# Kernel optimization log

Measured on AMD Instinct MI355X. Metric: run time of the kernel, lower is better.

The kernel has to match this reference:

```python
import jax, jax.numpy as jnp
import numpy as np

N = 32768      # total nodes (512 graphs x 64 padded nodes)
E = 262144     # edges (avg degree 8)
F_IN = 74      # atom feature dim
D0 = 128       # dim_embedding
D1 = 256       # hidden feats
B = 512        # batch_size (graphs)
NPG = 64       # nodes per graph
EPS = 1e-5     # BatchNorm1d eps


def setup_inputs() -> dict:
    key = jax.random.key(0)
    ks = jax.random.split(key, 8)
    def rn(k, shape, s=0.05):
        return jax.random.normal(k, shape, jnp.float32) * s
    # init_transform weight [D0, F_IN]; padding=True zeroes the last row
    W_init = rn(ks[0], (D0, F_IN)).at[-1].set(0.0)
    return {
        "node_feats": jax.random.normal(ks[1], (N, F_IN), jnp.float32),
        "W_init": W_init,
        "gcn_w1": rn(ks[2], (D0, D1)), "gcn_b1": jnp.zeros((D1,), jnp.float32),
        "res_w1": rn(ks[3], (D1, D0)), "res_b1": jnp.zeros((D1,), jnp.float32),
        "bn_g1": jnp.ones((D1,), jnp.float32), "bn_b1": jnp.zeros((D1,), jnp.float32),
        "gcn_w2": rn(ks[4], (D1, D1)), "gcn_b2": jnp.zeros((D1,), jnp.float32),
        "bn_g2": jnp.ones((D1,), jnp.float32), "bn_b2": jnp.zeros((D1,), jnp.float32),
        "edge_src": jax.random.randint(ks[5], (E,), 0, N),
        "edge_dst": jax.random.randint(ks[6], (E,), 0, N),
    }


def _agg(x, src, dst):
    # DGL GraphConv norm='both': D_out^{-1/2} gather-scatter D_in^{-1/2}, degrees clamped to >= 1
    ones = jnp.ones((src.shape[0],), x.dtype)
    deg_out = jnp.clip(jax.ops.segment_sum(ones, src, num_segments=N), 1.0)
    deg_in = jnp.clip(jax.ops.segment_sum(ones, dst, num_segments=N), 1.0)
    xs = x * jax.lax.rsqrt(deg_out)[:, None]
    agg = jax.ops.segment_sum(xs[src], dst, num_segments=N)  # [N, d]
    return agg * jax.lax.rsqrt(deg_in)[:, None]


def _bn(x, g, b):
    # BatchNorm1d training-mode: batch stats over node axis, biased var
    m = x.mean(0)
    v = x.var(0)
    return (x - m) * jax.lax.rsqrt(v + EPS) * g + b


def reference(node_feats, W_init, gcn_w1, gcn_b1, res_w1, res_b1, bn_g1, bn_b1,
              gcn_w2, gcn_b2, bn_g2, bn_b2, edge_src, edge_dst):
    h = node_feats @ W_init.T  # [N, D0]
    # layer 1: residual Linear 128->256, GCN(aggregate then weight, since in<out), GELU, BN
    res = h @ res_w1.T + res_b1
    g = jax.nn.gelu(_agg(h, edge_src, edge_dst) @ gcn_w1 + gcn_b1, approximate=False)
    h = _bn(g + res, bn_g1, bn_b1)
    # layer 2: Identity residual
    g = jax.nn.gelu(_agg(h, edge_src, edge_dst) @ gcn_w2 + gcn_b2, approximate=False)
    h = _bn(g + h, bn_g2, bn_b2)
    return h.reshape(B, NPG, D1)
```

## Files before the change

kernel.cpp:

```cpp
#include <hip/hip_runtime.h>
#include <hip/hip_bf16.h>
#include <math.h>

#define N_NODES 32768
#define E_EDGES 262144
#define F_INF   74
#define D0      128
#define D1      256
#define BN_EPS  1e-5f
#define RBLK    1024

typedef float f32x4 __attribute__((ext_vector_type(4)));
typedef short s16x8 __attribute__((ext_vector_type(8)));

__device__ __forceinline__ float b2f(ushort h) { return __uint_as_float(((unsigned)h) << 16); }
__device__ __forceinline__ ushort f2b(float f) {
    unsigned u = __float_as_uint(f);
    return (ushort)((u + 0x7FFFu + ((u >> 16) & 1u)) >> 16);
}
__device__ __forceinline__ float gelu_exact(float x) {
    return 0.5f * x * (1.0f + erff(x * 0.70710678118654752440f));
}


__global__ void k_degrees(const int* __restrict__ src, const int* __restrict__ dst,
                          int* __restrict__ deg) {
    int e = blockIdx.x * 256 + threadIdx.x;
    if (e < E_EDGES) {
        atomicAdd(&deg[src[e]], 1);
        atomicAdd(&deg[N_NODES + dst[e]], 1);
    }
}

__global__ __launch_bounds__(1024) void k_scan(const int* __restrict__ deg,
                                               int* __restrict__ row_off,
                                               float* __restrict__ rsq_out,
                                               float* __restrict__ rsq_in,
                                               int* __restrict__ cursor) {
    __shared__ int part[1024];
    int t = threadIdx.x;
    int base = t * 32;
    int loc[32];
    int s = 0;
    #pragma unroll
    for (int i = 0; i < 32; i++) { loc[i] = s; s += deg[N_NODES + base + i]; }
    part[t] = s;
    #pragma unroll
    for (int i = 0; i < 32; i++) {
        int n = base + i;
        int d_o = deg[n];           if (d_o < 1) d_o = 1;
        int d_i = deg[N_NODES + n]; if (d_i < 1) d_i = 1;
        rsq_out[n] = 1.0f / sqrtf((float)d_o);
        rsq_in[n]  = 1.0f / sqrtf((float)d_i);
        cursor[n] = 0;
    }
    __syncthreads();
    for (int off = 1; off < 1024; off <<= 1) {
        int v = 0;
        if (t >= off) v = part[t - off];
        __syncthreads();
        if (t >= off) part[t] += v;
        __syncthreads();
    }
    int pre = (t == 0) ? 0 : part[t - 1];
    #pragma unroll
    for (int i = 0; i < 32; i++) row_off[base + i] = pre + loc[i];
    if (t == 1023) row_off[N_NODES] = part[1023];
}

__global__ void k_fill(const int* __restrict__ src, const int* __restrict__ dst,
                       const int* __restrict__ row_off, int* __restrict__ cursor,
                       int* __restrict__ csr_src) {
    int e = blockIdx.x * 256 + threadIdx.x;
    if (e < E_EDGES) {
        int d = dst[e];
        int slot = atomicAdd(&cursor[d], 1);
        csr_src[row_off[d] + slot] = src[e];
    }
}

__global__ void k_prep(const float* __restrict__ Wi, const float* __restrict__ w1,
                       const float* __restrict__ rw, const float* __restrict__ w2,
                       float* __restrict__ WT, ushort* __restrict__ WB1,
                       ushort* __restrict__ RWB, ushort* __restrict__ WB2) {
    int idx = blockIdx.x * 256 + threadIdx.x;
    {
        int n = idx >> 8, k = idx & 255;
        WB2[idx] = f2b(w2[k * D1 + n]);
    }
    if (idx < D1 * D0) {
        int n = idx >> 7, k = idx & 127;
        WB1[idx] = f2b(w1[k * D1 + n]);
        RWB[idx] = f2b(rw[idx]);
    }
    if (idx < F_INF * D0) {
        int f = idx / D0, c = idx % D0;
        WT[f * D0 + c] = Wi[c * F_INF + f];
    }
}


__global__ __launch_bounds__(256) void k_init_gemm(
    const float* __restrict__ nf, const float* __restrict__ WT,
    ushort* __restrict__ h0) {
    __shared__ float sNF[64 * 76];
    int nb = blockIdx.x * 64;
    int tid = threadIdx.x;
    for (int idx = tid; idx < 64 * F_INF; idx += 256) {
        int row = idx / F_INF, f = idx % F_INF;
        sNF[row * 76 + f] = nf[(size_t)nb * F_INF + idx];
    }
    __syncthreads();
    int tc = tid & 31;
    int tn = tid >> 5;
    int c0 = tc * 4;
    float acc[8][4];
    #pragma unroll
    for (int i = 0; i < 8; i++)
        #pragma unroll
        for (int j = 0; j < 4; j++) acc[i][j] = 0.f;
    for (int k = 0; k < F_INF; k++) {
        float4 w = *reinterpret_cast<const float4*>(&WT[k * D0 + c0]);
        #pragma unroll
        for (int i = 0; i < 8; i++) {
            float a = sNF[(tn * 8 + i) * 76 + k];
            acc[i][0] += a * w.x; acc[i][1] += a * w.y;
            acc[i][2] += a * w.z; acc[i][3] += a * w.w;
        }
    }
    #pragma unroll
    for (int i = 0; i < 8; i++) {
        ushort4 o;
        o.x = f2b(acc[i][0]); o.y = f2b(acc[i][1]);
        o.z = f2b(acc[i][2]); o.w = f2b(acc[i][3]);
        *reinterpret_cast<ushort4*>(&h0[(size_t)(nb + tn * 8 + i) * D0 + c0]) = o;
    }
}


__global__ __launch_bounds__(512) void k_layer1f(
    const ushort* __restrict__ h0B,
    const float* __restrict__ rsq_out, const float* __restrict__ rsq_in,
    const int* __restrict__ row_off, const int* __restrict__ csr_src,
    const ushort* __restrict__ WB1, const ushort* __restrict__ RWB,
    const float* __restrict__ b1, const float* __restrict__ rb,
    ushort* __restrict__ t1B, float* __restrict__ partials) {
    __shared__ ushort sA[32 * 128];
    int tid = threadIdx.x;
    int rbase = blockIdx.x * 32;
    {
        int nloc = tid >> 4;
        int node = rbase + nloc;
        int f = (tid & 15) * 8;
        int beg = row_off[node], end = row_off[node + 1];
        float a[8];
        #pragma unroll
        for (int j = 0; j < 8; j++) a[j] = 0.f;
        int e = beg;
        for (; e + 3 < end; e += 4) {
            int s0 = csr_src[e], s1 = csr_src[e + 1], s2 = csr_src[e + 2], s3 = csr_src[e + 3];
            float c0 = rsq_out[s0], c1 = rsq_out[s1], c2 = rsq_out[s2], c3 = rsq_out[s3];
            s16x8 v0 = *reinterpret_cast<const s16x8*>(&h0B[(size_t)s0 * D0 + f]);
            s16x8 v1 = *reinterpret_cast<const s16x8*>(&h0B[(size_t)s1 * D0 + f]);
            s16x8 v2 = *reinterpret_cast<const s16x8*>(&h0B[(size_t)s2 * D0 + f]);
            s16x8 v3 = *reinterpret_cast<const s16x8*>(&h0B[(size_t)s3 * D0 + f]);
            #pragma unroll
            for (int j = 0; j < 8; j++)
                a[j] += b2f((ushort)v0[j]) * c0 + b2f((ushort)v1[j]) * c1 +
                        b2f((ushort)v2[j]) * c2 + b2f((ushort)v3[j]) * c3;
        }
        for (; e < end; e++) {
            int s = csr_src[e];
            float sc = rsq_out[s];
            s16x8 v = *reinterpret_cast<const s16x8*>(&h0B[(size_t)s * D0 + f]);
            #pragma unroll
            for (int j = 0; j < 8; j++) a[j] += b2f((ushort)v[j]) * sc;
        }
        float si = rsq_in[node];
        s16x8 o;
        #pragma unroll
        for (int j = 0; j < 8; j++) o[j] = (short)f2b(a[j] * si);
        int boff = nloc * 256 + ((f * 2) ^ ((nloc & 15) << 4));
        *reinterpret_cast<s16x8*>(((char*)sA) + boff) = o;
    }
    __syncthreads();
    int w = tid >> 6, lane = tid & 63, m = lane & 15, g4 = lane >> 4;
    int cb = w * 32;
    s16x8 BG[2][4], BR[2][4];
    #pragma unroll
    for (int nt = 0; nt < 2; nt++)
        #pragma unroll
        for (int j = 0; j < 4; j++) {
            BG[nt][j] = *reinterpret_cast<const s16x8*>(&WB1[(size_t)(cb + nt * 16 + m) * D0 + j * 32 + g4 * 8]);
            BR[nt][j] = *reinterpret_cast<const s16x8*>(&RWB[(size_t)(cb + nt * 16 + m) * D0 + j * 32 + g4 * 8]);
        }
    float bg[2], brv[2];
    #pragma unroll
    for (int nt = 0; nt < 2; nt++) {
        bg[nt]  = b1[cb + nt * 16 + m];
        brv[nt] = rb[cb + nt * 16 + m];
    }
    float ps[2] = {0.f, 0.f}, pq[2] = {0.f, 0.f};
    #pragma unroll
    for (int rt = 0; rt < 2; rt++) {
        int row = rt * 16 + m;
        s16x8 aA[4], aH[4];
        #pragma unroll
        for (int j = 0; j < 4; j++) {
            int boff = row * 256 + (((j * 4 + g4) * 16) ^ ((row & 15) << 4));
            aA[j] = *reinterpret_cast<const s16x8*>(((const char*)sA) + boff);
            aH[j] = *reinterpret_cast<const s16x8*>(&h0B[(size_t)(rbase + row) * D0 + j * 32 + g4 * 8]);
        }
        f32x4 accG[2], accR[2];
        #pragma unroll
        for (int nt = 0; nt < 2; nt++) {
            accG[nt] = (f32x4){0.f, 0.f, 0.f, 0.f};
            accR[nt] = (f32x4){0.f, 0.f, 0.f, 0.f};
        }
        #pragma unroll
        for (int j = 0; j < 4; j++)
            #pragma unroll
            for (int nt = 0; nt < 2; nt++) {
                accG[nt] = __builtin_amdgcn_mfma_f32_16x16x32_bf16(aA[j], BG[nt][j], accG[nt], 0, 0, 0);
                accR[nt] = __builtin_amdgcn_mfma_f32_16x16x32_bf16(aH[j], BR[nt][j], accR[nt], 0, 0, 0);
            }
        #pragma unroll
        for (int nt = 0; nt < 2; nt++) {
            int col = cb + nt * 16 + m;
            #pragma unroll
            for (int r = 0; r < 4; r++) {
                int orow = rbase + rt * 16 + g4 * 4 + r;
                float v = gelu_exact(accG[nt][r] + bg[nt]) + accR[nt][r] + brv[nt];
                t1B[(size_t)orow * D1 + col] = f2b(v);
                ps[nt] += v; pq[nt] += v * v;
            }
        }
    }
    #pragma unroll
    for (int nt = 0; nt < 2; nt++) {
        float s = ps[nt], q = pq[nt];
        s += __shfl_xor(s, 16); s += __shfl_xor(s, 32);
        q += __shfl_xor(q, 16); q += __shfl_xor(q, 32);
        if (g4 == 0) {
            int col = cb + nt * 16 + m;
            partials[(size_t)col * RBLK + blockIdx.x] = s;
            partials[(size_t)(256 + col) * RBLK + blockIdx.x] = q;
        }
    }
}


__global__ __launch_bounds__(512) void k_layer2f(
    const ushort* __restrict__ t1B,
    const float* __restrict__ sc1, const float* __restrict__ sh1,
    const float* __restrict__ rsq_out, const float* __restrict__ rsq_in,
    const int* __restrict__ row_off, const int* __restrict__ csr_src,
    const ushort* __restrict__ WB2, const float* __restrict__ b2,
    ushort* __restrict__ t2B, float* __restrict__ partials) {
    __shared__ ushort sA[32 * 256];
    int tid = threadIdx.x;
    int rbase = blockIdx.x * 32;
    {
        int nloc = tid >> 4;
        int node = rbase + nloc;
        int f0 = (tid & 15) * 8;
        int beg = row_off[node], end = row_off[node + 1];
        float a0[8], a1[8];
        #pragma unroll
        for (int j = 0; j < 8; j++) { a0[j] = 0.f; a1[j] = 0.f; }
        float ssum = 0.f;
        int e = beg;
        for (; e + 1 < end; e += 2) {
            int s0 = csr_src[e], s1 = csr_src[e + 1];
            float c0 = rsq_out[s0], c1 = rsq_out[s1];
            s16x8 v00 = *reinterpret_cast<const s16x8*>(&t1B[(size_t)s0 * D1 + f0]);
            s16x8 v01 = *reinterpret_cast<const s16x8*>(&t1B[(size_t)s0 * D1 + f0 + 128]);
            s16x8 v10 = *reinterpret_cast<const s16x8*>(&t1B[(size_t)s1 * D1 + f0]);
            s16x8 v11 = *reinterpret_cast<const s16x8*>(&t1B[(size_t)s1 * D1 + f0 + 128]);
            ssum += c0 + c1;
            #pragma unroll
            for (int j = 0; j < 8; j++) {
                a0[j] += b2f((ushort)v00[j]) * c0 + b2f((ushort)v10[j]) * c1;
                a1[j] += b2f((ushort)v01[j]) * c0 + b2f((ushort)v11[j]) * c1;
            }
        }
        for (; e < end; e++) {
            int s = csr_src[e];
            float sc = rsq_out[s];
            s16x8 v0 = *reinterpret_cast<const s16x8*>(&t1B[(size_t)s * D1 + f0]);
            s16x8 v1 = *reinterpret_cast<const s16x8*>(&t1B[(size_t)s * D1 + f0 + 128]);
            ssum += sc;
            #pragma unroll
            for (int j = 0; j < 8; j++) {
                a0[j] += b2f((ushort)v0[j]) * sc;
                a1[j] += b2f((ushort)v1[j]) * sc;
            }
        }
        float si = rsq_in[node];
        s16x8 o0, o1;
        #pragma unroll
        for (int j = 0; j < 8; j++) {
            o0[j] = (short)f2b((sc1[f0 + j] * a0[j] + sh1[f0 + j] * ssum) * si);
            o1[j] = (short)f2b((sc1[f0 + 128 + j] * a1[j] + sh1[f0 + 128 + j] * ssum) * si);
        }
        int swz = (nloc & 15) << 4;
        int b0 = nloc * 512 + ((f0 * 2) ^ swz);
        int b1_ = nloc * 512 + (((f0 + 128) * 2) ^ swz);
        *reinterpret_cast<s16x8*>(((char*)sA) + b0) = o0;
        *reinterpret_cast<s16x8*>(((char*)sA) + b1_) = o1;
    }
    __syncthreads();
    int w = tid >> 6, lane = tid & 63, m = lane & 15, g4 = lane >> 4;
    int cb = w * 32;
    s16x8 BG[2][8];
    #pragma unroll
    for (int nt = 0; nt < 2; nt++)
        #pragma unroll
        for (int j = 0; j < 8; j++)
            BG[nt][j] = *reinterpret_cast<const s16x8*>(&WB2[(size_t)(cb + nt * 16 + m) * D1 + j * 32 + g4 * 8]);
    float bg[2], a1c[2], s1c[2];
    #pragma unroll
    for (int nt = 0; nt < 2; nt++) {
        int col = cb + nt * 16 + m;
        bg[nt] = b2[col]; a1c[nt] = sc1[col]; s1c[nt] = sh1[col];
    }
    float ps[2] = {0.f, 0.f}, pq[2] = {0.f, 0.f};
    #pragma unroll
    for (int rt = 0; rt < 2; rt++) {
        int row = rt * 16 + m;
        s16x8 aA[8];
        #pragma unroll
        for (int j = 0; j < 8; j++) {
            int boff = row * 512 + (((j * 4 + g4) * 16) ^ ((row & 15) << 4));
            aA[j] = *reinterpret_cast<const s16x8*>(((const char*)sA) + boff);
        }
        f32x4 acc[2];
        #pragma unroll
        for (int nt = 0; nt < 2; nt++) acc[nt] = (f32x4){0.f, 0.f, 0.f, 0.f};
        #pragma unroll
        for (int j = 0; j < 8; j++)
            #pragma unroll
            for (int nt = 0; nt < 2; nt++)
                acc[nt] = __builtin_amdgcn_mfma_f32_16x16x32_bf16(aA[j], BG[nt][j], acc[nt], 0, 0, 0);
        #pragma unroll
        for (int nt = 0; nt < 2; nt++) {
            int col = cb + nt * 16 + m;
            #pragma unroll
            for (int r = 0; r < 4; r++) {
                int orow = rbase + rt * 16 + g4 * 4 + r;
                float h1v = fmaf(b2f(t1B[(size_t)orow * D1 + col]), a1c[nt], s1c[nt]);
                float v = gelu_exact(acc[nt][r] + bg[nt]) + h1v;
                t2B[(size_t)orow * D1 + col] = f2b(v);
                ps[nt] += v; pq[nt] += v * v;
            }
        }
    }
    #pragma unroll
    for (int nt = 0; nt < 2; nt++) {
        float s = ps[nt], q = pq[nt];
        s += __shfl_xor(s, 16); s += __shfl_xor(s, 32);
        q += __shfl_xor(q, 16); q += __shfl_xor(q, 32);
        if (g4 == 0) {
            int col = cb + nt * 16 + m;
            partials[(size_t)col * RBLK + blockIdx.x] = s;
            partials[(size_t)(256 + col) * RBLK + blockIdx.x] = q;
        }
    }
}


__global__ __launch_bounds__(256) void k_reduce(
    const float* __restrict__ partials, const float* __restrict__ g,
    const float* __restrict__ b, float* __restrict__ sc, float* __restrict__ sh) {
    int c = blockIdx.x;
    int t = threadIdx.x;
    const float* ps = partials + (size_t)c * RBLK;
    const float* pq = partials + (size_t)(256 + c) * RBLK;
    float s = ps[t] + ps[t + 256] + ps[t + 512] + ps[t + 768];
    float q = pq[t] + pq[t + 256] + pq[t + 512] + pq[t + 768];
    __shared__ float Ls[256], Lq[256];
    Ls[t] = s; Lq[t] = q;
    __syncthreads();
    for (int o = 128; o > 0; o >>= 1) {
        if (t < o) { Ls[t] += Ls[t + o]; Lq[t] += Lq[t + o]; }
        __syncthreads();
    }
    if (t == 0) {
        float m = Ls[0] * (1.0f / (float)N_NODES);
        float var = Lq[0] * (1.0f / (float)N_NODES) - m * m;
        float a = g[c] / sqrtf(var + BN_EPS);
        sc[c] = a;
        sh[c] = b[c] - m * a;
    }
}


__global__ __launch_bounds__(256) void k_apply(
    const ushort* __restrict__ t2B, const float* __restrict__ sc,
    const float* __restrict__ sh, float* __restrict__ out) {
    int idx = blockIdx.x * 256 + threadIdx.x;
    size_t base = (size_t)idx * 8;
    int c = (int)(base & 255);
    s16x8 v = *reinterpret_cast<const s16x8*>(&t2B[base]);
    float4 o0, o1;
    o0.x = fmaf(b2f((ushort)v[0]), sc[c + 0], sh[c + 0]);
    o0.y = fmaf(b2f((ushort)v[1]), sc[c + 1], sh[c + 1]);
    o0.z = fmaf(b2f((ushort)v[2]), sc[c + 2], sh[c + 2]);
    o0.w = fmaf(b2f((ushort)v[3]), sc[c + 3], sh[c + 3]);
    o1.x = fmaf(b2f((ushort)v[4]), sc[c + 4], sh[c + 4]);
    o1.y = fmaf(b2f((ushort)v[5]), sc[c + 5], sh[c + 5]);
    o1.z = fmaf(b2f((ushort)v[6]), sc[c + 6], sh[c + 6]);
    o1.w = fmaf(b2f((ushort)v[7]), sc[c + 7], sh[c + 7]);
    *reinterpret_cast<float4*>(&out[base]) = o0;
    *reinterpret_cast<float4*>(&out[base + 4]) = o1;
}


static inline size_t align256(size_t x) { return (x + 255) & ~(size_t)255; }

extern "C" void kernel_launch(void* const* d_in, const int* in_sizes, int n_in,
                              void* d_out, int out_size, void* d_ws, size_t ws_size,
                              hipStream_t stream) {
    const float* node_feats = (const float*)d_in[0];
    const float* W_init     = (const float*)d_in[1];
    const float* gcn_w1     = (const float*)d_in[2];
    const float* gcn_b1     = (const float*)d_in[3];
    const float* res_w1     = (const float*)d_in[4];
    const float* res_b1     = (const float*)d_in[5];
    const float* bn_g1      = (const float*)d_in[6];
    const float* bn_b1      = (const float*)d_in[7];
    const float* gcn_w2     = (const float*)d_in[8];
    const float* gcn_b2     = (const float*)d_in[9];
    const float* bn_g2      = (const float*)d_in[10];
    const float* bn_b2      = (const float*)d_in[11];
    const int*   edge_src   = (const int*)d_in[12];
    const int*   edge_dst   = (const int*)d_in[13];
    float* out = (float*)d_out;

    char* p = (char*)d_ws;
    size_t off = 0;
    auto take = [&](size_t bytes) { void* r = p + off; off += align256(bytes); return r; };

    ushort* h0B   = (ushort*)take((size_t)N_NODES * D0 * 2);
    ushort* t1B   = (ushort*)take((size_t)N_NODES * D1 * 2);
    ushort* t2B   = (ushort*)take((size_t)N_NODES * D1 * 2);
    float*  WT    = (float*)take((size_t)F_INF * D0 * 4);
    ushort* WB1   = (ushort*)take((size_t)D1 * D0 * 2);
    ushort* RWB   = (ushort*)take((size_t)D1 * D0 * 2);
    ushort* WB2   = (ushort*)take((size_t)D1 * D1 * 2);
    float*  part1 = (float*)take((size_t)2 * 256 * RBLK * 4);
    float*  part2 = (float*)take((size_t)2 * 256 * RBLK * 4);
    float*  sc1   = (float*)take(256 * 4);
    float*  sh1   = (float*)take(256 * 4);
    float*  sc2   = (float*)take(256 * 4);
    float*  sh2   = (float*)take(256 * 4);
    float*  rsq_out = (float*)take((size_t)N_NODES * 4);
    float*  rsq_in  = (float*)take((size_t)N_NODES * 4);
    int*    degi    = (int*)take((size_t)2 * N_NODES * 4);
    int*    cursor  = (int*)take((size_t)N_NODES * 4);
    int*    row_off = (int*)take((size_t)(N_NODES + 2) * 4);
    int*    csr_src = (int*)take((size_t)E_EDGES * 4);

    hipMemsetAsync(degi, 0, (size_t)2 * N_NODES * 4, stream);

    k_degrees<<<(E_EDGES + 255) / 256, 256, 0, stream>>>(edge_src, edge_dst, degi);
    k_scan<<<1, 1024, 0, stream>>>(degi, row_off, rsq_out, rsq_in, cursor);
    k_fill<<<(E_EDGES + 255) / 256, 256, 0, stream>>>(edge_src, edge_dst, row_off, cursor, csr_src);

    k_prep<<<(D1 * D1) / 256, 256, 0, stream>>>(W_init, gcn_w1, res_w1, gcn_w2, WT, WB1, RWB, WB2);

    k_init_gemm<<<N_NODES / 64, 256, 0, stream>>>(node_feats, WT, h0B);

    k_layer1f<<<RBLK, 512, 0, stream>>>(h0B, rsq_out, rsq_in, row_off, csr_src,
                                        WB1, RWB, gcn_b1, res_b1, t1B, part1);
    k_reduce<<<256, 256, 0, stream>>>(part1, bn_g1, bn_b1, sc1, sh1);

    k_layer2f<<<RBLK, 512, 0, stream>>>(t1B, sc1, sh1, rsq_out, rsq_in, row_off, csr_src,
                                        WB2, gcn_b2, t2B, part2);
    k_reduce<<<256, 256, 0, stream>>>(part2, bn_g2, bn_b2, sc2, sh2);

    k_apply<<<(N_NODES * D1 / 8) / 256, 256, 0, stream>>>(t2B, sc2, sh2, out);
}
```

Measured before the change: 218.5 us.

## Use MFMA for init projection, precompute per-edge scales, prefetch residual

Replaces the scalar FP32 init GEMM with a bf16 MFMA kernel. The node features and init weight are converted and zero-padded to K=96 in the prep kernel. The CSR fill also stores a per-edge rsq_out scale, so both aggregation loops read it contiguously instead of doing a random gather. Layer 2 loads its residual values into registers before the MFMA loop. The costs are an extra bf16 copy of the node features, an extra edge array, and reduced precision for the init projection.

```diff
diff --git a/kernel.cpp b/kernel.cpp
--- a/kernel.cpp
+++ b/kernel.cpp
@@ -5,6 +5,7 @@
 #define N_NODES 32768
 #define E_EDGES 262144
 #define F_INF   74
+#define KP      96
 #define D0      128
 #define D1      256
 #define BN_EPS  1e-5f
@@ -69,79 +70,76 @@
 }
 
 __global__ void k_fill(const int* __restrict__ src, const int* __restrict__ dst,
-                       const int* __restrict__ row_off, int* __restrict__ cursor,
-                       int* __restrict__ csr_src) {
+                       const int* __restrict__ row_off, const float* __restrict__ rsq_out,
+                       int* __restrict__ cursor, int* __restrict__ csr_src,
+                       float* __restrict__ esc) {
     int e = blockIdx.x * 256 + threadIdx.x;
     if (e < E_EDGES) {
         int d = dst[e];
+        int s = src[e];
         int slot = atomicAdd(&cursor[d], 1);
-        csr_src[row_off[d] + slot] = src[e];
-    }
-}
-
-__global__ void k_prep(const float* __restrict__ Wi, const float* __restrict__ w1,
-                       const float* __restrict__ rw, const float* __restrict__ w2,
-                       float* __restrict__ WT, ushort* __restrict__ WB1,
-                       ushort* __restrict__ RWB, ushort* __restrict__ WB2) {
+        int pos = row_off[d] + slot;
+        csr_src[pos] = s;
+        esc[pos] = rsq_out[s];
+    }
+}
+
+
+__global__ void k_prep(const float* __restrict__ nf, const float* __restrict__ Wi,
+                       const float* __restrict__ w1, const float* __restrict__ rw,
+                       const float* __restrict__ w2,
+                       ushort* __restrict__ nfB, ushort* __restrict__ WTB,
+                       ushort* __restrict__ WB1, ushort* __restrict__ RWB,
+                       ushort* __restrict__ WB2) {
     int idx = blockIdx.x * 256 + threadIdx.x;
     {
-        int n = idx >> 8, k = idx & 255;
-        WB2[idx] = f2b(w2[k * D1 + n]);
+        int n = idx / KP, k = idx - n * KP;
+        nfB[idx] = (k < F_INF) ? f2b(nf[n * F_INF + k]) : (ushort)0;
+    }
+    if (idx < D0 * KP) {
+        int c = idx / KP, k = idx - c * KP;
+        WTB[idx] = (k < F_INF) ? f2b(Wi[c * F_INF + k]) : (ushort)0;
     }
     if (idx < D1 * D0) {
         int n = idx >> 7, k = idx & 127;
         WB1[idx] = f2b(w1[k * D1 + n]);
         RWB[idx] = f2b(rw[idx]);
     }
-    if (idx < F_INF * D0) {
-        int f = idx / D0, c = idx % D0;
-        WT[f * D0 + c] = Wi[c * F_INF + f];
-    }
-}
-
-
-__global__ __launch_bounds__(256) void k_init_gemm(
-    const float* __restrict__ nf, const float* __restrict__ WT,
+    if (idx < D1 * D1) {
+        int n = idx >> 8, k = idx & 255;
+        WB2[idx] = f2b(w2[k * D1 + n]);
+    }
+}
+
+
+__global__ __launch_bounds__(512) void k_init_mfma(
+    const ushort* __restrict__ nfB, const ushort* __restrict__ WTB,
     ushort* __restrict__ h0) {
-    __shared__ float sNF[64 * 76];
-    int nb = blockIdx.x * 64;
     int tid = threadIdx.x;
-    for (int idx = tid; idx < 64 * F_INF; idx += 256) {
-        int row = idx / F_INF, f = idx % F_INF;
-        sNF[row * 76 + f] = nf[(size_t)nb * F_INF + idx];
-    }
-    __syncthreads();
-    int tc = tid & 31;
-    int tn = tid >> 5;
-    int c0 = tc * 4;
-    float acc[8][4];
-    #pragma unroll
-    for (int i = 0; i < 8; i++)
-        #pragma unroll
-        for (int j = 0; j < 4; j++) acc[i][j] = 0.f;
-    for (int k = 0; k < F_INF; k++) {
-        float4 w = *reinterpret_cast<const float4*>(&WT[k * D0 + c0]);
-        #pragma unroll
-        for (int i = 0; i < 8; i++) {
-            float a = sNF[(tn * 8 + i) * 76 + k];
-            acc[i][0] += a * w.x; acc[i][1] += a * w.y;
-            acc[i][2] += a * w.z; acc[i][3] += a * w.w;
-        }
-    }
-    #pragma unroll
-    for (int i = 0; i < 8; i++) {
-        ushort4 o;
-        o.x = f2b(acc[i][0]); o.y = f2b(acc[i][1]);
-        o.z = f2b(acc[i][2]); o.w = f2b(acc[i][3]);
-        *reinterpret_cast<ushort4*>(&h0[(size_t)(nb + tn * 8 + i) * D0 + c0]) = o;
-    }
+    int w = tid >> 6, lane = tid & 63, m = lane & 15, g4 = lane >> 4;
+    int col = w * 16 + m;
+    int rbase = blockIdx.x * 16;
+    s16x8 B[3], A[3];
+    #pragma unroll
+    for (int j = 0; j < 3; j++)
+        B[j] = *reinterpret_cast<const s16x8*>(&WTB[(size_t)col * KP + j * 32 + g4 * 8]);
+    #pragma unroll
+    for (int j = 0; j < 3; j++)
+        A[j] = *reinterpret_cast<const s16x8*>(&nfB[(size_t)(rbase + m) * KP + j * 32 + g4 * 8]);
+    f32x4 acc = (f32x4){0.f, 0.f, 0.f, 0.f};
+    #pragma unroll
+    for (int j = 0; j < 3; j++)
+        acc = __builtin_amdgcn_mfma_f32_16x16x32_bf16(A[j], B[j], acc, 0, 0, 0);
+    #pragma unroll
+    for (int r = 0; r < 4; r++)
+        h0[(size_t)(rbase + g4 * 4 + r) * D0 + col] = f2b(acc[r]);
 }
 
 
 __global__ __launch_bounds__(512) void k_layer1f(
-    const ushort* __restrict__ h0B,
-    const float* __restrict__ rsq_out, const float* __restrict__ rsq_in,
+    const ushort* __restrict__ h0B, const float* __restrict__ rsq_in,
     const int* __restrict__ row_off, const int* __restrict__ csr_src,
+    const float* __restrict__ esc,
     const ushort* __restrict__ WB1, const ushort* __restrict__ RWB,
     const float* __restrict__ b1, const float* __restrict__ rb,
     ushort* __restrict__ t1B, float* __restrict__ partials) {
@@ -159,7 +157,7 @@
         int e = beg;
         for (; e + 3 < end; e += 4) {
             int s0 = csr_src[e], s1 = csr_src[e + 1], s2 = csr_src[e + 2], s3 = csr_src[e + 3];
-            float c0 = rsq_out[s0], c1 = rsq_out[s1], c2 = rsq_out[s2], c3 = rsq_out[s3];
+            float c0 = esc[e], c1 = esc[e + 1], c2 = esc[e + 2], c3 = esc[e + 3];
             s16x8 v0 = *reinterpret_cast<const s16x8*>(&h0B[(size_t)s0 * D0 + f]);
             s16x8 v1 = *reinterpret_cast<const s16x8*>(&h0B[(size_t)s1 * D0 + f]);
             s16x8 v2 = *reinterpret_cast<const s16x8*>(&h0B[(size_t)s2 * D0 + f]);
@@ -171,7 +169,7 @@
         }
         for (; e < end; e++) {
             int s = csr_src[e];
-            float sc = rsq_out[s];
+            float sc = esc[e];
             s16x8 v = *reinterpret_cast<const s16x8*>(&h0B[(size_t)s * D0 + f]);
             #pragma unroll
             for (int j = 0; j < 8; j++) a[j] += b2f((ushort)v[j]) * sc;
@@ -253,8 +251,9 @@
 __global__ __launch_bounds__(512) void k_layer2f(
     const ushort* __restrict__ t1B,
     const float* __restrict__ sc1, const float* __restrict__ sh1,
-    const float* __restrict__ rsq_out, const float* __restrict__ rsq_in,
+    const float* __restrict__ rsq_in,
     const int* __restrict__ row_off, const int* __restrict__ csr_src,
+    const float* __restrict__ esc,
     const ushort* __restrict__ WB2, const float* __restrict__ b2,
     ushort* __restrict__ t2B, float* __restrict__ partials) {
     __shared__ ushort sA[32 * 256];
@@ -272,7 +271,7 @@
         int e = beg;
         for (; e + 1 < end; e += 2) {
             int s0 = csr_src[e], s1 = csr_src[e + 1];
-            float c0 = rsq_out[s0], c1 = rsq_out[s1];
+            float c0 = esc[e], c1 = esc[e + 1];
             s16x8 v00 = *reinterpret_cast<const s16x8*>(&t1B[(size_t)s0 * D1 + f0]);
             s16x8 v01 = *reinterpret_cast<const s16x8*>(&t1B[(size_t)s0 * D1 + f0 + 128]);
             s16x8 v10 = *reinterpret_cast<const s16x8*>(&t1B[(size_t)s1 * D1 + f0]);
@@ -286,7 +285,7 @@
         }
         for (; e < end; e++) {
             int s = csr_src[e];
-            float sc = rsq_out[s];
+            float sc = esc[e];
             s16x8 v0 = *reinterpret_cast<const s16x8*>(&t1B[(size_t)s * D1 + f0]);
             s16x8 v1 = *reinterpret_cast<const s16x8*>(&t1B[(size_t)s * D1 + f0 + 128]);
             ssum += sc;
@@ -312,6 +311,16 @@
     __syncthreads();
     int w = tid >> 6, lane = tid & 63, m = lane & 15, g4 = lane >> 4;
     int cb = w * 32;
+    ushort rres[2][2][4];
+    #pragma unroll
+    for (int nt = 0; nt < 2; nt++) {
+        int col = cb + nt * 16 + m;
+        #pragma unroll
+        for (int rt = 0; rt < 2; rt++)
+            #pragma unroll
+            for (int r = 0; r < 4; r++)
+                rres[nt][rt][r] = t1B[(size_t)(rbase + rt * 16 + g4 * 4 + r) * D1 + col];
+    }
     s16x8 BG[2][8];
     #pragma unroll
     for (int nt = 0; nt < 2; nt++)
@@ -348,7 +357,7 @@
             #pragma unroll
             for (int r = 0; r < 4; r++) {
                 int orow = rbase + rt * 16 + g4 * 4 + r;
-                float h1v = fmaf(b2f(t1B[(size_t)orow * D1 + col]), a1c[nt], s1c[nt]);
+                float h1v = fmaf(b2f(rres[nt][rt][r]), a1c[nt], s1c[nt]);
                 float v = gelu_exact(acc[nt][r] + bg[nt]) + h1v;
                 t2B[(size_t)orow * D1 + col] = f2b(v);
                 ps[nt] += v; pq[nt] += v * v;
@@ -444,7 +453,8 @@
     ushort* h0B   = (ushort*)take((size_t)N_NODES * D0 * 2);
     ushort* t1B   = (ushort*)take((size_t)N_NODES * D1 * 2);
     ushort* t2B   = (ushort*)take((size_t)N_NODES * D1 * 2);
-    float*  WT    = (float*)take((size_t)F_INF * D0 * 4);
+    ushort* nfB   = (ushort*)take((size_t)N_NODES * KP * 2);
+    ushort* WTB   = (ushort*)take((size_t)D0 * KP * 2);
     ushort* WB1   = (ushort*)take((size_t)D1 * D0 * 2);
     ushort* RWB   = (ushort*)take((size_t)D1 * D0 * 2);
     ushort* WB2   = (ushort*)take((size_t)D1 * D1 * 2);
@@ -460,22 +470,25 @@
     int*    cursor  = (int*)take((size_t)N_NODES * 4);
     int*    row_off = (int*)take((size_t)(N_NODES + 2) * 4);
     int*    csr_src = (int*)take((size_t)E_EDGES * 4);
+    float*  esc     = (float*)take((size_t)E_EDGES * 4);
 
     hipMemsetAsync(degi, 0, (size_t)2 * N_NODES * 4, stream);
 
     k_degrees<<<(E_EDGES + 255) / 256, 256, 0, stream>>>(edge_src, edge_dst, degi);
     k_scan<<<1, 1024, 0, stream>>>(degi, row_off, rsq_out, rsq_in, cursor);
-    k_fill<<<(E_EDGES + 255) / 256, 256, 0, stream>>>(edge_src, edge_dst, row_off, cursor, csr_src);
-
-    k_prep<<<(D1 * D1) / 256, 256, 0, stream>>>(W_init, gcn_w1, res_w1, gcn_w2, WT, WB1, RWB, WB2);
-
-    k_init_gemm<<<N_NODES / 64, 256, 0, stream>>>(node_feats, WT, h0B);
-
-    k_layer1f<<<RBLK, 512, 0, stream>>>(h0B, rsq_out, rsq_in, row_off, csr_src,
+    k_fill<<<(E_EDGES + 255) / 256, 256, 0, stream>>>(edge_src, edge_dst, row_off, rsq_out,
+                                                      cursor, csr_src, esc);
+
+    k_prep<<<(N_NODES * KP) / 256, 256, 0, stream>>>(node_feats, W_init, gcn_w1, res_w1, gcn_w2,
+                                                     nfB, WTB, WB1, RWB, WB2);
+
+    k_init_mfma<<<N_NODES / 16, 512, 0, stream>>>(nfB, WTB, h0B);
+
+    k_layer1f<<<RBLK, 512, 0, stream>>>(h0B, rsq_in, row_off, csr_src, esc,
                                         WB1, RWB, gcn_b1, res_b1, t1B, part1);
     k_reduce<<<256, 256, 0, stream>>>(part1, bn_g1, bn_b1, sc1, sh1);
 
-    k_layer2f<<<RBLK, 512, 0, stream>>>(t1B, sc1, sh1, rsq_out, rsq_in, row_off, csr_src,
+    k_layer2f<<<RBLK, 512, 0, stream>>>(t1B, sc1, sh1, rsq_in, row_off, csr_src, esc,
                                         WB2, gcn_b2, t2B, part2);
     k_reduce<<<256, 256, 0, stream>>>(part2, bn_g2, bn_b2, sc2, sh2);
 
```

New measurement: 219.1 us. Within noise of the previous version (+0.2%).
